# Optimization experiments

Hardware: AMD Instinct MI355X
Metric: run time of the kernel (lower is better)

## Reference

```python
import jax, jax.numpy as jnp
import numpy as np

IN_F = 2048
OUT_F = 8192
NUM_BLOCKS = 2097152  # (IN_F*OUT_F)//8
K = 4096
BLOCK = 8

def setup_inputs() -> dict:
    key = jax.random.key(0)
    k1, k2, k3, k4 = jax.random.split(key, 4)
    x = jax.random.normal(k1, (4, 2048, IN_F), dtype=jnp.float32)
    codebook = jax.random.normal(k2, (K, BLOCK), dtype=jnp.float32)
    indices = jax.random.randint(k3, (NUM_BLOCKS,), 0, K, dtype=jnp.int64)
    bias = jax.random.normal(k4, (OUT_F,), dtype=jnp.float32)
    return {"x": x, "codebook": codebook, "indices": indices, "bias": bias}

def reference(x, codebook, indices, bias):
    # Dequantize: gather codewords and reassemble the full weight matrix.
    # codebook[indices]: (num_blocks, block) -> flatten -> (in_f, out_f)
    W = codebook[indices].reshape(IN_F, OUT_F)
    # GPT-2 Conv1D: out = x @ W + b  (W is (in, out), not transposed)
    out = jnp.matmul(x, W) + bias
    return out
```

## Files before the change

### kernel.cpp

```cpp
#include <hip/hip_runtime.h>
#include <hip/hip_bf16.h>

typedef unsigned short ushort_t;
typedef __attribute__((ext_vector_type(8))) short short8;
typedef __attribute__((ext_vector_type(4))) float f32x4;

#define M_DIM 8192
#define N_DIM 8192
#define K_DIM 2048
#define BM 256
#define BN 256
#define BK 32
#define NT (K_DIM / BK)
#define SLOT (BM * BK)
#define KROW64 ((size_t)64 * K_DIM)

__device__ __forceinline__ ushort_t f2bf(float f) {
    union { float f; unsigned u; } v; v.f = f;
    unsigned r = v.u + 0x7fffu + ((v.u >> 16) & 1u);
    return (ushort_t)(r >> 16);
}

__device__ __forceinline__ void async_copy16(const void* g, void* l) {
    __builtin_amdgcn_global_load_lds(
        (const __attribute__((address_space(1))) void*)g,
        (__attribute__((address_space(3))) void*)l, 16, 0, 0);
}

#define BAR() __builtin_amdgcn_s_barrier()
#define LGKM(n) do { asm volatile("s_waitcnt lgkmcnt(" #n ")" ::: "memory"); \
                     __builtin_amdgcn_sched_barrier(0); } while (0)
#define VMC(n) asm volatile("s_waitcnt vmcnt(" #n ")" ::: "memory")

__global__ __launch_bounds__(256) void convert_x(const float* __restrict__ x,
                                                 ushort_t* __restrict__ A) {
    int t = blockIdx.x * 256 + threadIdx.x;
    const float4* p = (const float4*)x + (size_t)t * 2;
    float4 a = p[0], b = p[1];
    short8 o;
    o[0] = (short)f2bf(a.x); o[1] = (short)f2bf(a.y);
    o[2] = (short)f2bf(a.z); o[3] = (short)f2bf(a.w);
    o[4] = (short)f2bf(b.x); o[5] = (short)f2bf(b.y);
    o[6] = (short)f2bf(b.z); o[7] = (short)f2bf(b.w);
    *(short8*)(A + (size_t)t * 8) = o;
}

__global__ __launch_bounds__(256) void dequant_wt(const int* __restrict__ indices,
                                                  const float* __restrict__ codebook,
                                                  ushort_t* __restrict__ Bt) {
    int g = blockIdx.x;
    int i = blockIdx.y * 256 + threadIdx.x;
    int idx = indices[(size_t)i * 1024 + g];
    const float4* cb = (const float4*)(codebook + (size_t)idx * 8);
    float4 lo = cb[0], hi = cb[1];
    size_t base = (size_t)g * 8 * K_DIM + i;
    Bt[base + 0 * K_DIM] = f2bf(lo.x);
    Bt[base + 1 * K_DIM] = f2bf(lo.y);
    Bt[base + 2 * K_DIM] = f2bf(lo.z);
    Bt[base + 3 * K_DIM] = f2bf(lo.w);
    Bt[base + 4 * K_DIM] = f2bf(hi.x);
    Bt[base + 5 * K_DIM] = f2bf(hi.y);
    Bt[base + 6 * K_DIM] = f2bf(hi.z);
    Bt[base + 7 * K_DIM] = f2bf(hi.w);
}

__device__ __forceinline__ void read8(const char* p, int rd, short8 (&fr)[8]) {
#pragma unroll
    for (int i = 0; i < 8; ++i)
        fr[i] = *(const short8*)(p + rd + i * 1024);
}

__device__ __forceinline__ void mfma64(const short8 (&af)[8], const short8 (&bf)[8],
                                       f32x4 (&acc)[8][8]) {
    __builtin_amdgcn_s_setprio(1);
#pragma unroll
    for (int i = 0; i < 8; ++i)
#pragma unroll
        for (int j = 0; j < 8; ++j)
            acc[i][j] = __builtin_amdgcn_mfma_f32_16x16x32_bf16(
                af[i], bf[j], acc[i][j], 0, 0, 0);
    __builtin_amdgcn_s_setprio(0);
}

__global__ __launch_bounds__(256, 1) void gemm_pipe4(const ushort_t* __restrict__ A,
                                                     const ushort_t* __restrict__ Bt,
                                                     const float* __restrict__ bias,
                                                     float* __restrict__ C) {
    __shared__ __align__(16) ushort_t lds_a[4][SLOT];
    __shared__ __align__(16) ushort_t lds_b[4][SLOT];

    const int bid = blockIdx.x;
    const int xc = bid & 7;
    const int qq = bid >> 3;
    const int mt = ((xc >> 1) << 2) + (qq & 3) + (((qq >> 5) & 1) << 4);
    const int nt = ((xc & 1) << 3) + ((qq >> 2) & 7) + (((qq >> 6) & 1) << 4);
    const int m0 = mt * BM;
    const int n0 = nt * BN;

    const int tid = threadIdx.x;
    const int lane = tid & 63;
    const int wid = tid >> 6;
    const int wm = wid >> 1, wn = wid & 1;
    const int lane15 = lane & 15, laneq = lane >> 4;

    const int rdA = (wm * 128 + lane15) * 64 + ((laneq ^ (lane15 & 3)) << 4);
    const int rdB = (wn * 128 + lane15) * 64 + ((laneq ^ (lane15 & 3)) << 4);

    const int r = tid >> 2;
    const int cg = (tid & 3) ^ (r & 3);
    const ushort_t* Ab = A  + (size_t)(m0 + r) * K_DIM + cg * 8;
    const ushort_t* Bb = Bt + (size_t)(n0 + r) * K_DIM + cg * 8;
    const int dq = tid * 16;

#define STAGE(t) do { \
        const int _sl = (t) & 3; \
        char* _da = (char*)&lds_a[_sl][0] + dq; \
        char* _db = (char*)&lds_b[_sl][0] + dq; \
        const ushort_t* _ga = Ab + (size_t)(t) * BK; \
        const ushort_t* _gb = Bb + (size_t)(t) * BK; \
        async_copy16(_ga,              _da); \
        async_copy16(_ga + KROW64,     _da + 4096); \
        async_copy16(_ga + 2 * KROW64, _da + 8192); \
        async_copy16(_ga + 3 * KROW64, _da + 12288); \
        async_copy16(_gb,              _db); \
        async_copy16(_gb + KROW64,     _db + 4096); \
        async_copy16(_gb + 2 * KROW64, _db + 8192); \
        async_copy16(_gb + 3 * KROW64, _db + 12288); \
    } while (0)

    f32x4 acc[8][8];
#pragma unroll
    for (int i = 0; i < 8; ++i)
#pragma unroll
        for (int j = 0; j < 8; ++j) acc[i][j] = (f32x4){0.f, 0.f, 0.f, 0.f};

    short8 afC[8], bfC[8], afN[8], bfN[8];

    STAGE(0); STAGE(1); STAGE(2);
    VMC(8);
    BAR();
    read8((const char*)&lds_a[0][0], rdA, afC);
    read8((const char*)&lds_b[0][0], rdB, bfC);

#define PHASE_MAIN(p, AC, BC, AN, BN) do { \
        read8((const char*)&lds_a[((p) + 1) & 3][0], rdA, AN); \
        read8((const char*)&lds_b[((p) + 1) & 3][0], rdB, BN); \
        STAGE((p) + 3); \
        LGKM(15); \
        mfma64(AC, BC, acc); \
        VMC(8); \
        BAR(); \
    } while (0)

    for (int p = 0; p < 60; p += 2) {
        PHASE_MAIN(p,     afC, bfC, afN, bfN);
        PHASE_MAIN(p + 1, afN, bfN, afC, bfC);
    }
    read8((const char*)&lds_a[61 & 3][0], rdA, afN);
    read8((const char*)&lds_b[61 & 3][0], rdB, bfN);
    STAGE(63);
    LGKM(15); mfma64(afC, bfC, acc); VMC(8); BAR();
    read8((const char*)&lds_a[62 & 3][0], rdA, afC);
    read8((const char*)&lds_b[62 & 3][0], rdB, bfC);
    LGKM(15); mfma64(afN, bfN, acc); VMC(0); BAR();
    read8((const char*)&lds_a[63 & 3][0], rdA, afN);
    read8((const char*)&lds_b[63 & 3][0], rdB, bfN);
    LGKM(15); mfma64(afC, bfC, acc); BAR();
    LGKM(0); mfma64(afN, bfN, acc);

#pragma unroll
    for (int jg = 0; jg < 8; ++jg) {
        const int col = n0 + wn * 128 + jg * 16 + lane15;
        const float bv = bias[col];
#pragma unroll
        for (int ig = 0; ig < 8; ++ig) {
            const int row = m0 + wm * 128 + ig * 16 + laneq * 4;
            f32x4 v = acc[ig][jg];
#pragma unroll
            for (int q2 = 0; q2 < 4; ++q2)
                C[(size_t)(row + q2) * N_DIM + col] = v[q2] + bv;
        }
    }
#undef STAGE
#undef PHASE_MAIN
}

extern "C" void kernel_launch(void* const* d_in, const int* in_sizes, int n_in,
                              void* d_out, int out_size, void* d_ws, size_t ws_size,
                              hipStream_t stream) {
    const float* x = (const float*)d_in[0];
    const float* codebook = (const float*)d_in[1];
    const int* indices = (const int*)d_in[2];
    const float* bias = (const float*)d_in[3];
    float* out = (float*)d_out;

    ushort_t* A  = (ushort_t*)d_ws;
    ushort_t* Bt = (ushort_t*)d_ws + (size_t)M_DIM * K_DIM;

    convert_x<<<dim3(M_DIM * K_DIM / (256 * 8)), 256, 0, stream>>>(x, A);
    dequant_wt<<<dim3(1024, 8), 256, 0, stream>>>(indices, codebook, Bt);
    gemm_pipe4<<<dim3((M_DIM / BM) * (N_DIM / BN)), 256, 0, stream>>>(A, Bt, bias, out);
}
```

Before: 335.6 us.

## Split GEMM tile across eight waves with new LDS swizzle layout

The 256x256 GEMM tile moves from 4 waves (each 128x128) to 8 waves (each 128x64), using 512 threads with a launch bound allowing 2 blocks per CU. Accumulator registers per wave are halved, and the LDS read/write swizzle and async-copy row mapping are redesigned for the new 128-byte row layout. A scheduling barrier is also added after vmcnt waits. The aim is more waves in flight to hide latency, at the cost of more LDS reads per MFMA and more barrier participants.

```diff
diff --git a/kernel.cpp b/kernel.cpp
--- a/kernel.cpp
+++ b/kernel.cpp
@@ -12,8 +12,7 @@
 #define BN 256
 #define BK 32
 #define NT (K_DIM / BK)
-#define SLOT (BM * BK)
-#define KROW64 ((size_t)64 * K_DIM)
+#define SLOTE 8192
 
 __device__ __forceinline__ ushort_t f2bf(float f) {
     union { float f; unsigned u; } v; v.f = f;
@@ -30,7 +29,8 @@
 #define BAR() __builtin_amdgcn_s_barrier()
 #define LGKM(n) do { asm volatile("s_waitcnt lgkmcnt(" #n ")" ::: "memory"); \
                      __builtin_amdgcn_sched_barrier(0); } while (0)
-#define VMC(n) asm volatile("s_waitcnt vmcnt(" #n ")" ::: "memory")
+#define VMC(n) do { asm volatile("s_waitcnt vmcnt(" #n ")" ::: "memory"); \
+                    __builtin_amdgcn_sched_barrier(0); } while (0)
 
 __global__ __launch_bounds__(256) void convert_x(const float* __restrict__ x,
                                                  ushort_t* __restrict__ A) {
@@ -70,24 +70,30 @@
         fr[i] = *(const short8*)(p + rd + i * 1024);
 }
 
-__device__ __forceinline__ void mfma64(const short8 (&af)[8], const short8 (&bf)[8],
-                                       f32x4 (&acc)[8][8]) {
+__device__ __forceinline__ void read4(const char* p, int rd, short8 (&fr)[4]) {
+#pragma unroll
+    for (int j = 0; j < 4; ++j)
+        fr[j] = *(const short8*)(p + rd + j * 1024);
+}
+
+__device__ __forceinline__ void mfma32(const short8 (&af)[8], const short8 (&bf)[4],
+                                       f32x4 (&acc)[8][4]) {
     __builtin_amdgcn_s_setprio(1);
 #pragma unroll
     for (int i = 0; i < 8; ++i)
 #pragma unroll
-        for (int j = 0; j < 8; ++j)
+        for (int j = 0; j < 4; ++j)
             acc[i][j] = __builtin_amdgcn_mfma_f32_16x16x32_bf16(
                 af[i], bf[j], acc[i][j], 0, 0, 0);
     __builtin_amdgcn_s_setprio(0);
 }
 
-__global__ __launch_bounds__(256, 1) void gemm_pipe4(const ushort_t* __restrict__ A,
-                                                     const ushort_t* __restrict__ Bt,
-                                                     const float* __restrict__ bias,
-                                                     float* __restrict__ C) {
-    __shared__ __align__(16) ushort_t lds_a[4][SLOT];
-    __shared__ __align__(16) ushort_t lds_b[4][SLOT];
+__global__ __launch_bounds__(512, 2) void gemm_ra8(const ushort_t* __restrict__ A,
+                                                   const ushort_t* __restrict__ Bt,
+                                                   const float* __restrict__ bias,
+                                                   float* __restrict__ C) {
+    __shared__ __align__(16) ushort_t lds_a[4][SLOTE];
+    __shared__ __align__(16) ushort_t lds_b[4][SLOTE];
 
     const int bid = blockIdx.x;
     const int xc = bid & 7;
@@ -100,77 +106,74 @@
     const int tid = threadIdx.x;
     const int lane = tid & 63;
     const int wid = tid >> 6;
-    const int wm = wid >> 1, wn = wid & 1;
+    const int wm = wid >> 2, wn = wid & 3;
     const int lane15 = lane & 15, laneq = lane >> 4;
 
-    const int rdA = (wm * 128 + lane15) * 64 + ((laneq ^ (lane15 & 3)) << 4);
-    const int rdB = (wn * 128 + lane15) * 64 + ((laneq ^ (lane15 & 3)) << 4);
-
-    const int r = tid >> 2;
-    const int cg = (tid & 3) ^ (r & 3);
-    const ushort_t* Ab = A  + (size_t)(m0 + r) * K_DIM + cg * 8;
-    const ushort_t* Bb = Bt + (size_t)(n0 + r) * K_DIM + cg * 8;
+    const int l2 = lane15 >> 1;
+    const int gsw = (((((lane15 & 1) << 2) | laneq) ^ l2) << 4);
+    const int rdA = (wm * 64 + l2) * 128 + gsw;
+    const int rdB = (wn * 32 + l2) * 128 + gsw;
+
+    const int e = (tid & 7) ^ ((tid >> 3) & 7);
+    const int kgs = e & 3;
+    const int row0 = ((tid >> 3) << 1) + ((e >> 2) & 1);
+    const ushort_t* Ab = A  + (size_t)(m0 + row0) * K_DIM + kgs * 8;
+    const ushort_t* Bb = Bt + (size_t)(n0 + row0) * K_DIM + kgs * 8;
     const int dq = tid * 16;
-
-#define STAGE(t) do { \
-        const int _sl = (t) & 3; \
+    const size_t R128 = (size_t)128 * K_DIM;
+
+#define STAGE(t) do { const int _sl = (t) & 3; \
         char* _da = (char*)&lds_a[_sl][0] + dq; \
         char* _db = (char*)&lds_b[_sl][0] + dq; \
         const ushort_t* _ga = Ab + (size_t)(t) * BK; \
         const ushort_t* _gb = Bb + (size_t)(t) * BK; \
-        async_copy16(_ga,              _da); \
-        async_copy16(_ga + KROW64,     _da + 4096); \
-        async_copy16(_ga + 2 * KROW64, _da + 8192); \
-        async_copy16(_ga + 3 * KROW64, _da + 12288); \
-        async_copy16(_gb,              _db); \
-        async_copy16(_gb + KROW64,     _db + 4096); \
-        async_copy16(_gb + 2 * KROW64, _db + 8192); \
-        async_copy16(_gb + 3 * KROW64, _db + 12288); \
+        async_copy16(_ga,        _da); \
+        async_copy16(_ga + R128, _da + 8192); \
+        async_copy16(_gb,        _db); \
+        async_copy16(_gb + R128, _db + 8192); \
     } while (0)
 
-    f32x4 acc[8][8];
+    f32x4 acc[8][4];
 #pragma unroll
     for (int i = 0; i < 8; ++i)
 #pragma unroll
-        for (int j = 0; j < 8; ++j) acc[i][j] = (f32x4){0.f, 0.f, 0.f, 0.f};
-
-    short8 afC[8], bfC[8], afN[8], bfN[8];
+        for (int j = 0; j < 4; ++j) acc[i][j] = (f32x4){0.f, 0.f, 0.f, 0.f};
+
+    short8 afC[8], afN[8], bfC[4], bfN[4];
 
     STAGE(0); STAGE(1); STAGE(2);
-    VMC(8);
+    VMC(4);
     BAR();
     read8((const char*)&lds_a[0][0], rdA, afC);
-    read8((const char*)&lds_b[0][0], rdB, bfC);
-
-#define PHASE_MAIN(p, AC, BC, AN, BN) do { \
+    read4((const char*)&lds_b[0][0], rdB, bfC);
+
+#define PHASE(p, AC, BC, AN, BN_) do { \
         read8((const char*)&lds_a[((p) + 1) & 3][0], rdA, AN); \
-        read8((const char*)&lds_b[((p) + 1) & 3][0], rdB, BN); \
+        read4((const char*)&lds_b[((p) + 1) & 3][0], rdB, BN_); \
         STAGE((p) + 3); \
-        LGKM(15); \
-        mfma64(AC, BC, acc); \
-        VMC(8); \
+        LGKM(12); \
+        mfma32(AC, BC, acc); \
+        VMC(4); \
         BAR(); \
     } while (0)
 
     for (int p = 0; p < 60; p += 2) {
-        PHASE_MAIN(p,     afC, bfC, afN, bfN);
-        PHASE_MAIN(p + 1, afN, bfN, afC, bfC);
+        PHASE(p,     afC, bfC, afN, bfN);
+        PHASE(p + 1, afN, bfN, afC, bfC);
     }
-    read8((const char*)&lds_a[61 & 3][0], rdA, afN);
-    read8((const char*)&lds_b[61 & 3][0], rdB, bfN);
-    STAGE(63);
-    LGKM(15); mfma64(afC, bfC, acc); VMC(8); BAR();
+    PHASE(60, afC, bfC, afN, bfN);
     read8((const char*)&lds_a[62 & 3][0], rdA, afC);
-    read8((const char*)&lds_b[62 & 3][0], rdB, bfC);
-    LGKM(15); mfma64(afN, bfN, acc); VMC(0); BAR();
+    read4((const char*)&lds_b[62 & 3][0], rdB, bfC);
+    LGKM(12); mfma32(afN, bfN, acc); VMC(0); BAR();
     read8((const char*)&lds_a[63 & 3][0], rdA, afN);
-    read8((const char*)&lds_b[63 & 3][0], rdB, bfN);
-    LGKM(15); mfma64(afC, bfC, acc); BAR();
-    LGKM(0); mfma64(afN, bfN, acc);
-
-#pragma unroll
-    for (int jg = 0; jg < 8; ++jg) {
-        const int col = n0 + wn * 128 + jg * 16 + lane15;
+    read4((const char*)&lds_b[63 & 3][0], rdB, bfN);
+    LGKM(12); mfma32(afC, bfC, acc); BAR();
+    LGKM(0); mfma32(afN, bfN, acc);
+#undef PHASE
+
+#pragma unroll
+    for (int jg = 0; jg < 4; ++jg) {
+        const int col = n0 + wn * 64 + jg * 16 + lane15;
         const float bv = bias[col];
 #pragma unroll
         for (int ig = 0; ig < 8; ++ig) {
@@ -182,7 +185,6 @@
         }
     }
 #undef STAGE
-#undef PHASE_MAIN
 }
 
 extern "C" void kernel_launch(void* const* d_in, const int* in_sizes, int n_in,
@@ -199,5 +201,5 @@
 
     convert_x<<<dim3(M_DIM * K_DIM / (256 * 8)), 256, 0, stream>>>(x, A);
     dequant_wt<<<dim3(1024, 8), 256, 0, stream>>>(indices, codebook, Bt);
-    gemm_pipe4<<<dim3((M_DIM / BM) * (N_DIM / BN)), 256, 0, stream>>>(A, Bt, bias, out);
-}
+    gemm_ra8<<<dim3((M_DIM / BM) * (N_DIM / BN)), 512, 0, stream>>>(A, Bt, bias, out);
+}
```

Result: faster. 310.7 us (-7.4%).
